# Kernel tuning notes

Measured on AMD Instinct MI355X. Metric: run time of the kernel, lower is better.

Reference implementation:

```python
import jax, jax.numpy as jnp
import numpy as np

B, N = 32, 50000
E = 200000
D, D_LG = 64, 256
M_ALL, M_MEM = 100000, 80000
NUM_VI_SEG = 80000


def _dense(key, din, dout):
    k1, k2 = jax.random.split(key)
    lim = 1.0 / np.sqrt(din)
    W = jax.random.uniform(k1, (din, dout), jnp.float32, -lim, lim)
    b = jax.random.uniform(k2, (dout,), jnp.float32, -lim, lim)
    return W, b


def setup_inputs() -> dict:
    key = jax.random.key(0)
    ks = jax.random.split(key, 16)
    rng = np.random.RandomState(0)

    eg = np.sort(rng.randint(0, B, E)).astype(np.int32)
    vi = rng.randint(0, N, E).astype(np.int32)
    vj = rng.randint(0, N, E).astype(np.int32)
    rel = rng.randint(0, 200, E).astype(np.int32)
    seg_vi = np.sort(rng.randint(0, NUM_VI_SEG, E)).astype(np.int32)
    seg_vj = rng.randint(0, E, E).astype(np.int32)
    e2vi = rng.randint(0, M_ALL, E).astype(np.int32)
    e2vj = rng.randint(0, M_ALL, E).astype(np.int32)
    scanned_edges = jnp.asarray(np.stack([eg, vi, vj, rel, seg_vi, seg_vj, e2vi, e2vj], axis=1))

    new_idx = np.sort(rng.choice(M_ALL, M_MEM, replace=False)).astype(np.int32)[:, None]

    W_h, b_h = _dense(ks[0], D, D)
    W_hlg, b_hlg = _dense(ks[1], D_LG, D)
    W_rlg, b_rlg = _dense(ks[2], D_LG, D)
    Wl0, bl0 = _dense(ks[3], D, D)
    Wr0, br0 = _dense(ks[4], D, D)
    Wl1, bl1 = _dense(ks[5], 2 * D, D)
    Wr1, br1 = _dense(ks[6], 2 * D, D)

    return {
        'node_attention': jax.random.uniform(ks[7], (B, N), jnp.float32),
        'edges_y': jax.random.uniform(ks[8], (E,), jnp.float32),
        'hidden_uncon': jax.random.normal(ks[9], (1, N, D_LG), jnp.float32),
        'hidden_con': jax.random.normal(ks[10], (M_MEM, D), jnp.float32),
        'query_head_emb': jax.random.normal(ks[11], (B, D_LG), jnp.float32),
        'query_rel_emb': jax.random.normal(ks[12], (B, D_LG), jnp.float32),
        'W_h': W_h, 'b_h': b_h, 'W_hlg': W_hlg, 'b_hlg': b_hlg,
        'W_rlg': W_rlg, 'b_rlg': b_rlg,
        'Wl0': Wl0, 'bl0': bl0, 'Wr0': Wr0, 'br0': br0,
        'Wl1': Wl1, 'bl1': bl1, 'Wr1': Wr1, 'br1': br1,
        'scanned_edges': scanned_edges,
        'new_idx_for_memorized': jnp.asarray(new_idx),
        'n_memorized_and_scanned_nodes': M_ALL,
    }


def _segment_softmax(logits, seg, num_seg):
    # numerically-stable sparse softmax over sorted vi-segments
    m = jax.ops.segment_max(logits, seg, num_segments=num_seg)
    e = jnp.exp(logits - m[seg])
    s = jax.ops.segment_sum(e, seg, num_segments=num_seg)
    return e / s[seg]


def reference(node_attention, edges_y, hidden_uncon, hidden_con,
              query_head_emb, query_rel_emb,
              W_h, b_h, W_hlg, b_hlg, W_rlg, b_rlg,
              Wl0, bl0, Wr0, br0, Wl1, bl1, Wr1, br1,
              scanned_edges, new_idx_for_memorized, n_memorized_and_scanned_nodes):
    Bv, Nv = node_attention.shape
    eg = scanned_edges[:, 0]
    vi = scanned_edges[:, 1]
    vj = scanned_edges[:, 2]
    seg_vi = scanned_edges[:, 4]
    e2vi = scanned_edges[:, 6]
    e2vj = scanned_edges[:, 7]

    # proj_for_hidden, scatter memorized states to memorized+scanned slots
    hc = jnp.tanh(hidden_con @ W_h + b_h)                        # M_mem x D
    hc_full = jnp.zeros((n_memorized_and_scanned_nodes, hc.shape[-1]), hc.dtype)
    hc_full = hc_full.at[new_idx_for_memorized[:, 0]].set(hc)    # M_all x D

    hu = jnp.tanh(hidden_uncon @ W_hlg + b_hlg)
    qh = jnp.tanh(query_head_emb @ W_hlg + b_hlg)                # B x D (use_ent_emb)
    qr = jnp.tanh(query_rel_emb @ W_rlg + b_rlg)                 # B x D
    qv = qh + qr

    # node2edge gathers (context = conditioned + unconditioned hidden)
    h_vi = hc_full[e2vi] + hu[0, vi]                             # E x D
    h_vj = hc_full[e2vj] + hu[0, vj]                             # E x D
    q_e = qv[eg]                                                 # E x D

    # transition_fn G with interact [[[0],[1]], [[0,2],[1,2]]]
    l0 = jnp.tanh(h_vi @ Wl0 + bl0)
    r0 = jnp.tanh(h_vj @ Wr0 + br0)
    l1 = jnp.tanh(jnp.concatenate([h_vi, q_e], -1) @ Wl1 + bl1)
    r1 = jnp.tanh(jnp.concatenate([h_vj, q_e], -1) @ Wr1 + br1)
    logits = jnp.sum(l0 * r0, -1) + jnp.sum(l1 * r1, -1)         # E

    # neighbor softmax at vi, modulated by edges_y
    trans = _segment_softmax(logits, seg_vi, NUM_VI_SEG) * edges_y

    # flow: gather attention at vi, aggregate(sum) scatter to (eg_idx, vj)
    flow = node_attention[eg, vi] * trans
    new_att = jnp.zeros((Bv, Nv), flow.dtype).at[eg, vj].add(flow)
    return new_att
```

## Files before the change

### kernel.cpp

```cpp
#include <hip/hip_runtime.h>


typedef __attribute__((ext_vector_type(8))) short s16x8;
typedef __attribute__((ext_vector_type(4))) float f32x4;
typedef __attribute__((ext_vector_type(8))) unsigned short u16x8;

__device__ __forceinline__ float fast_tanh(float x) {
    float e = __expf(2.0f * x);
    return 1.0f - 2.0f * __builtin_amdgcn_rcpf(e + 1.0f);
}

__device__ __forceinline__ unsigned short bf16r(float f) {
    unsigned int u = __float_as_uint(f);
    u = (u + 0x7fffu + ((u >> 16) & 1u)) >> 16;
    return (unsigned short)u;
}
__device__ __forceinline__ float bf16f(unsigned short h) {
    return __uint_as_float(((unsigned int)h) << 16);
}
__device__ __forceinline__ float blo(unsigned int u) {
    return __uint_as_float(u << 16);
}
__device__ __forceinline__ float bhi(unsigned int u) {
    return __uint_as_float(u & 0xffff0000u);
}

__device__ __forceinline__ int saddr(int row, int chunk) {
    return (row << 6) + ((chunk ^ (row & 7)) << 2);
}

__global__ void k_scatter_inv(const int* __restrict__ new_idx, int* __restrict__ inv, int M) {
    int i = blockIdx.x * blockDim.x + threadIdx.x;
    if (i < M) inv[new_idx[i]] = i;
}

__global__ void k_pack(const float* __restrict__ Wl0, const float* __restrict__ Wl1,
                       const float* __restrict__ Wr0, const float* __restrict__ Wr1,
                       unsigned short* __restrict__ Bp) {
    int tid = blockIdx.x * blockDim.x + threadIdx.x;
    if (tid >= 2048) return;
    int lane = tid & 63;
    int ks = (tid >> 6) & 1;
    int g = tid >> 7;
    int col = g * 16 + (lane & 15);
    int kb = ks * 32 + (lane >> 4) * 8;
    const float* W = (col < 64) ? Wl0 : (col < 128) ? Wl1 : (col < 192) ? Wr0 : Wr1;
    int c = col & 63;
    #pragma unroll
    for (int i = 0; i < 8; ++i) {
        float w = W[(kb + i) * 64 + c];
        unsigned short hi = bf16r(w);
        unsigned short lo = bf16r(w - bf16f(hi));
        Bp[(size_t)tid * 8 + i] = hi;
        Bp[16384 + (size_t)tid * 8 + i] = lo;
    }
}

__global__ void k_q(const float* __restrict__ qhe, const float* __restrict__ qre,
                    const float* __restrict__ W_hlg, const float* __restrict__ b_hlg,
                    const float* __restrict__ W_rlg, const float* __restrict__ b_rlg,
                    const float* __restrict__ Wl1, const float* __restrict__ bl1,
                    const float* __restrict__ Wr1, const float* __restrict__ br1,
                    float* __restrict__ ql1b, float* __restrict__ qr1b) {
    __shared__ float qv_s[64];
    int b = blockIdx.x, d = threadIdx.x;
    float ah = 0.f, ar = 0.f;
    for (int k = 0; k < 256; ++k) {
        ah += qhe[b * 256 + k] * W_hlg[k * 64 + d];
        ar += qre[b * 256 + k] * W_rlg[k * 64 + d];
    }
    qv_s[d] = fast_tanh(ah + b_hlg[d]) + fast_tanh(ar + b_rlg[d]);
    __syncthreads();
    float a1 = 0.f, a2 = 0.f;
    for (int k = 0; k < 64; ++k) {
        float v = qv_s[k];
        a1 += v * Wl1[(64 + k) * 64 + d];
        a2 += v * Wr1[(64 + k) * 64 + d];
    }
    ql1b[b * 64 + d] = a1 + bl1[d];
    qr1b[b * 64 + d] = a2 + br1[d];
}

__global__ __launch_bounds__(256, 6) void k_tab(
        const float* __restrict__ Xc, const float* __restrict__ Xu,
        const float* __restrict__ W_h, const float* __restrict__ b_h,
        const float* __restrict__ W_hlg, const float* __restrict__ b_hlg,
        const float* __restrict__ bl0, const float* __restrict__ br0,
        const unsigned short* __restrict__ Bp,
        unsigned short* __restrict__ Ahc, unsigned short* __restrict__ Ahu,
        int M, int N, int HCB) {
    __shared__ float s[64 * 64];
    __shared__ unsigned short dstage[16 * 264];
    unsigned short* hhi = reinterpret_cast<unsigned short*>(s);

    const int t = threadIdx.x;
    const int wu = __builtin_amdgcn_readfirstlane(t >> 6);
    const int lane = t & 63;
    const bool hc = ((int)blockIdx.x < HCB);

    float acc1[16];
    #pragma unroll
    for (int c = 0; c < 16; ++c) acc1[c] = 0.f;

    int base, rows;
    const float* bias;
    unsigned short* table;

    if (hc) {
        base = blockIdx.x * 64;
        rows = (M - base < 64) ? (M - base) : 64;
        bias = b_h;
        table = Ahc;
        #pragma unroll
        for (int i = 0; i < 4; ++i) {
            int f = i * 256 + t;
            int r = f >> 4, ch = f & 15;
            float4 v = make_float4(0.f, 0.f, 0.f, 0.f);
            if (r < rows) v = *reinterpret_cast<const float4*>(Xc + (size_t)(base + r) * 64 + (ch << 2));
            *reinterpret_cast<float4*>(&s[saddr(r, ch)]) = v;
        }
        __syncthreads();
        for (int k4 = 0; k4 < 16; ++k4) {
            float4 xv = *reinterpret_cast<const float4*>(&s[saddr(lane, k4)]);
            #pragma unroll
            for (int kk = 0; kk < 4; ++kk) {
                float xk = (&xv.x)[kk];
                const float* wrow = W_h + (k4 * 4 + kk) * 64 + wu * 16;
                #pragma unroll
                for (int c = 0; c < 16; ++c) acc1[c] = __builtin_fmaf(xk, wrow[c], acc1[c]);
            }
        }
    } else {
        base = ((int)blockIdx.x - HCB) * 64;
        rows = (N - base < 64) ? (N - base) : 64;
        bias = b_hlg;
        table = Ahu;
        float4 xr[4];
        #pragma unroll
        for (int i = 0; i < 4; ++i) {
            int f = i * 256 + t;
            int r = f >> 4, ch = f & 15;
            xr[i] = make_float4(0.f, 0.f, 0.f, 0.f);
            if (r < rows)
                xr[i] = *reinterpret_cast<const float4*>(Xu + (size_t)(base + r) * 256 + (ch << 2));
        }
        for (int kc = 0; kc < 4; ++kc) {
            __syncthreads();
            #pragma unroll
            for (int i = 0; i < 4; ++i) {
                int f = i * 256 + t;
                int r = f >> 4, ch = f & 15;
                *reinterpret_cast<float4*>(&s[saddr(r, ch)]) = xr[i];
            }
            __syncthreads();
            if (kc + 1 < 4) {
                #pragma unroll
                for (int i = 0; i < 4; ++i) {
                    int f = i * 256 + t;
                    int r = f >> 4, ch = f & 15;
                    if (r < rows)
                        xr[i] = *reinterpret_cast<const float4*>(
                            Xu + (size_t)(base + r) * 256 + (kc + 1) * 64 + (ch << 2));
                }
            }
            const float* Wb = W_hlg + (size_t)kc * 64 * 64;
            for (int k4 = 0; k4 < 16; ++k4) {
                float4 xv = *reinterpret_cast<const float4*>(&s[saddr(lane, k4)]);
                #pragma unroll
                for (int kk = 0; kk < 4; ++kk) {
                    float xk = (&xv.x)[kk];
                    const float* wrow = Wb + (k4 * 4 + kk) * 64 + wu * 16;
                    #pragma unroll
                    for (int c = 0; c < 16; ++c) acc1[c] = __builtin_fmaf(xk, wrow[c], acc1[c]);
                }
            }
        }
    }

    __syncthreads();
    {
        unsigned short hi[16];
        #pragma unroll
        for (int c = 0; c < 16; ++c)
            hi[c] = bf16r(fast_tanh(acc1[c] + bias[wu * 16 + c]));
        int o = lane * 68 + wu * 16;
        #pragma unroll
        for (int c = 0; c < 16; ++c) hhi[o + c] = hi[c];
    }
    __syncthreads();

    const s16x8* Bph = reinterpret_cast<const s16x8*>(Bp);
    const s16x8* Bpl = reinterpret_cast<const s16x8*>(Bp + 16384);
    const int l15 = lane & 15, l4 = lane >> 4;
    for (int rt = 0; rt < 4; ++rt) {
        int arow = (rt * 16 + l15) * 68 + l4 * 8;
        s16x8 a0v = *reinterpret_cast<const s16x8*>(&hhi[arow]);
        s16x8 a1v = *reinterpret_cast<const s16x8*>(&hhi[arow + 32]);
        #pragma unroll
        for (int ct = 0; ct < 4; ++ct) {
            int g = wu * 4 + ct;
            s16x8 bh0 = Bph[(g * 2 + 0) * 64 + lane];
            s16x8 bh1 = Bph[(g * 2 + 1) * 64 + lane];
            s16x8 bl0v = Bpl[(g * 2 + 0) * 64 + lane];
            s16x8 bl1v = Bpl[(g * 2 + 1) * 64 + lane];
            f32x4 acc = {0.f, 0.f, 0.f, 0.f};
            acc = __builtin_amdgcn_mfma_f32_16x16x32_bf16(a0v, bh0, acc, 0, 0, 0);
            acc = __builtin_amdgcn_mfma_f32_16x16x32_bf16(a1v, bh1, acc, 0, 0, 0);
            acc = __builtin_amdgcn_mfma_f32_16x16x32_bf16(a0v, bl0v, acc, 0, 0, 0);
            acc = __builtin_amdgcn_mfma_f32_16x16x32_bf16(a1v, bl1v, acc, 0, 0, 0);
            float badd = 0.f;
            if (!hc) {
                if (g < 4) badd = bl0[g * 16 + l15];
                else if (g >= 8 && g < 12) badd = br0[(g - 8) * 16 + l15];
            }
            int side = g >> 3, which = (g >> 2) & 1;
            int x = (g & 3) * 16 + l15;
            int pos = side * 128 + x * 2 + which;
            #pragma unroll
            for (int r = 0; r < 4; ++r)
                dstage[(l4 * 4 + r) * 264 + pos] = bf16r(acc[r] + badd);
        }
        __syncthreads();
        #pragma unroll
        for (int it = 0; it < 2; ++it) {
            int f = (it * 256 + t) * 8;
            int row = f >> 8, off = f & 255;
            u16x8 v = *reinterpret_cast<const u16x8*>(&dstage[row * 264 + off]);
            int grow = rt * 16 + row;
            if (grow < rows)
                *reinterpret_cast<u16x8*>(&table[(size_t)(base + grow) * 256 + off]) = v;
        }
        __syncthreads();
    }
}

__global__ void k_edge(const int* __restrict__ se, const int* __restrict__ inv,
                       const unsigned int* __restrict__ Ahc, const unsigned int* __restrict__ Ahu,
                       const float* __restrict__ ql1b, const float* __restrict__ qr1b,
                       float* __restrict__ trans, float* __restrict__ psum,
                       int E, int ZROW) {
    int tid = blockIdx.x * blockDim.x + threadIdx.x;
    int e = tid >> 4;
    int sl = tid & 15;
    if (e >= E) return;
    const int4* sr = reinterpret_cast<const int4*>(se + (size_t)e * 8);
    int4 ra = sr[0], rb = sr[1];
    int eg = ra.x, vi = ra.y, vj = ra.z, seg = rb.x, e2vi = rb.z, e2vj = rb.w;
    int ii = inv[e2vi]; ii = (ii < 0) ? ZROW : ii;
    int ij = inv[e2vj]; ij = (ij < 0) ? ZROW : ij;
    uint4 a  = *reinterpret_cast<const uint4*>(Ahc + (size_t)ii * 128 + sl * 4);
    uint4 b  = *reinterpret_cast<const uint4*>(Ahu + (size_t)vi * 128 + sl * 4);
    uint4 c  = *reinterpret_cast<const uint4*>(Ahc + (size_t)ij * 128 + 64 + sl * 4);
    uint4 d4 = *reinterpret_cast<const uint4*>(Ahu + (size_t)vj * 128 + 64 + sl * 4);
    float4 q1 = *reinterpret_cast<const float4*>(ql1b + eg * 64 + sl * 4);
    float4 q2 = *reinterpret_cast<const float4*>(qr1b + eg * 64 + sl * 4);
    float acc = 0.f;
    #pragma unroll
    for (int j = 0; j < 4; ++j) {
        unsigned int av = (&a.x)[j], bv = (&b.x)[j];
        unsigned int cv = (&c.x)[j], dv = (&d4.x)[j];
        float l0 = fast_tanh(blo(av) + blo(bv));
        float l1 = fast_tanh(bhi(av) + bhi(bv) + (&q1.x)[j]);
        float r0 = fast_tanh(blo(cv) + blo(dv));
        float r1 = fast_tanh(bhi(cv) + bhi(dv) + (&q2.x)[j]);
        acc = __builtin_fmaf(l0, r0, acc);
        acc = __builtin_fmaf(l1, r1, acc);
    }
    #pragma unroll
    for (int off = 8; off; off >>= 1) acc += __shfl_xor(acc, off);
    if (sl == 0) {
        float ex = __expf(acc);
        trans[e] = ex;
        atomicAdd(&psum[seg], ex);
    }
}

__global__ void k_final(const int* __restrict__ se, const float* __restrict__ trans,
                        const float* __restrict__ psum, const float* __restrict__ ey,
                        const float* __restrict__ natt, float* __restrict__ out,
                        int E, int N) {
    int e = blockIdx.x * blockDim.x + threadIdx.x;
    if (e >= E) return;
    const int* row = se + (size_t)e * 8;
    int eg = row[0], vi = row[1], vj = row[2], seg = row[4];
    float t = trans[e] * __builtin_amdgcn_rcpf(psum[seg]) * ey[e] * natt[(size_t)eg * N + vi];
    atomicAdd(&out[(size_t)eg * N + vj], t);
}

extern "C" void kernel_launch(void* const* d_in, const int* in_sizes, int n_in,
                              void* d_out, int out_size, void* d_ws, size_t ws_size,
                              hipStream_t stream) {
    const float* natt  = (const float*)d_in[0];
    const float* ey    = (const float*)d_in[1];
    const float* h_unc = (const float*)d_in[2];
    const float* h_con = (const float*)d_in[3];
    const float* qhe   = (const float*)d_in[4];
    const float* qre   = (const float*)d_in[5];
    const float* W_h   = (const float*)d_in[6];
    const float* b_h   = (const float*)d_in[7];
    const float* W_hlg = (const float*)d_in[8];
    const float* b_hlg = (const float*)d_in[9];
    const float* W_rlg = (const float*)d_in[10];
    const float* b_rlg = (const float*)d_in[11];
    const float* Wl0   = (const float*)d_in[12];
    const float* bl0   = (const float*)d_in[13];
    const float* Wr0   = (const float*)d_in[14];
    const float* br0   = (const float*)d_in[15];
    const float* Wl1   = (const float*)d_in[16];
    const float* bl1   = (const float*)d_in[17];
    const float* Wr1   = (const float*)d_in[18];
    const float* br1   = (const float*)d_in[19];
    const int* se      = (const int*)d_in[20];
    const int* new_idx = (const int*)d_in[21];

    const int B     = 32;
    const int N     = in_sizes[0] / B;
    const int E     = in_sizes[20] / 8;
    const int M_MEM = in_sizes[21];
    const int M_ALL = 100000;
    const int NSEG  = 80000;

    char* ws = (char*)d_ws;
    size_t off = 0;
    unsigned short* Ahc = (unsigned short*)(ws + off);  off += (size_t)(M_MEM + 1) * 256 * 2;
    unsigned short* Ahu = (unsigned short*)(ws + off);  off += (size_t)N * 256 * 2;
    int* inv = (int*)(ws + off);            off += (size_t)M_ALL * 4;
    float* trans = (float*)(ws + off);      off += (size_t)E * 4;
    float* psum = (float*)(ws + off);       off += (size_t)NSEG * 4;
    float* ql1b = (float*)(ws + off);       off += (size_t)B * 64 * 4;
    float* qr1b = (float*)(ws + off);       off += (size_t)B * 64 * 4;
    unsigned short* Bpack = (unsigned short*)(ws + off); off += (size_t)2 * 16384 * 2;

    hipMemsetAsync(d_out, 0, (size_t)out_size * 4, stream);
    hipMemsetAsync(inv, 0xFF, (size_t)M_ALL * 4, stream);
    hipMemsetAsync(psum, 0, (size_t)NSEG * 4, stream);
    hipMemsetAsync(Ahc + (size_t)M_MEM * 256, 0, 256 * 2, stream);

    const int HCB = (M_MEM + 63) / 64;
    const int HUB = (N + 63) / 64;

    k_scatter_inv<<<(M_MEM + 255) / 256, 256, 0, stream>>>(new_idx, inv, M_MEM);
    k_pack<<<8, 256, 0, stream>>>(Wl0, Wl1, Wr0, Wr1, Bpack);
    k_q<<<B, 64, 0, stream>>>(qhe, qre, W_hlg, b_hlg, W_rlg, b_rlg,
                              Wl1, bl1, Wr1, br1, ql1b, qr1b);
    k_tab<<<HCB + HUB, 256, 0, stream>>>(h_con, h_unc, W_h, b_h, W_hlg, b_hlg,
                                         bl0, br0, Bpack, Ahc, Ahu, M_MEM, N, HCB);
    k_edge<<<((size_t)E * 16 + 255) / 256, 256, 0, stream>>>(se, inv, (const unsigned int*)Ahc,
                                                (const unsigned int*)Ahu, ql1b, qr1b,
                                                trans, psum, E, M_MEM);
    k_final<<<(E + 255) / 256, 256, 0, stream>>>(se, trans, psum, ey, natt, (float*)d_out, E, N);
}
```

Measured before the change: 141.7 us.

## Move edge-weight gathers into edge kernel and batch LDS loads in table GEMM

The edge kernel now multiplies the exponentiated logit by edges_y and the gathered node attention, and writes a compact (output index, segment) pair per edge. The final kernel then reads only that pair, the partial value and the segment sum, and no longer re-reads the 32-byte edge row or does the random node-attention gather. The first-stage GEMM in the table kernel also loads four LDS rows at once before the FMAs, to give the scheduler more independent loads. In exchange the edge kernel does an extra scattered gather and writes an additional 8-byte array per edge.

```diff
diff --git a/kernel.cpp b/kernel.cpp
--- a/kernel.cpp
+++ b/kernel.cpp
@@ -81,6 +81,25 @@
     qr1b[b * 64 + d] = a2 + br1[d];
 }
 
+__device__ __forceinline__ void s1_batch(const float* __restrict__ s, int lane, int b4,
+                                         const float* __restrict__ Wbase, int wu,
+                                         float acc1[16]) {
+    f32x4 xrow[4];
+    #pragma unroll
+    for (int j = 0; j < 4; ++j)
+        xrow[j] = *reinterpret_cast<const f32x4*>(&s[saddr(lane, b4 * 4 + j)]);
+    #pragma unroll
+    for (int k4 = 0; k4 < 4; ++k4) {
+        #pragma unroll
+        for (int kk = 0; kk < 4; ++kk) {
+            float xk = xrow[k4][kk];
+            const float* wrow = Wbase + ((b4 * 4 + k4) * 4 + kk) * 64 + wu * 16;
+            #pragma unroll
+            for (int c = 0; c < 16; ++c) acc1[c] = __builtin_fmaf(xk, wrow[c], acc1[c]);
+        }
+    }
+}
+
 __global__ __launch_bounds__(256, 6) void k_tab(
         const float* __restrict__ Xc, const float* __restrict__ Xu,
         const float* __restrict__ W_h, const float* __restrict__ b_h,
@@ -120,16 +139,8 @@
             *reinterpret_cast<float4*>(&s[saddr(r, ch)]) = v;
         }
         __syncthreads();
-        for (int k4 = 0; k4 < 16; ++k4) {
-            float4 xv = *reinterpret_cast<const float4*>(&s[saddr(lane, k4)]);
-            #pragma unroll
-            for (int kk = 0; kk < 4; ++kk) {
-                float xk = (&xv.x)[kk];
-                const float* wrow = W_h + (k4 * 4 + kk) * 64 + wu * 16;
-                #pragma unroll
-                for (int c = 0; c < 16; ++c) acc1[c] = __builtin_fmaf(xk, wrow[c], acc1[c]);
-            }
-        }
+        for (int b4 = 0; b4 < 4; ++b4)
+            s1_batch(s, lane, b4, W_h, wu, acc1);
     } else {
         base = ((int)blockIdx.x - HCB) * 64;
         rows = (N - base < 64) ? (N - base) : 64;
@@ -164,16 +175,8 @@
                 }
             }
             const float* Wb = W_hlg + (size_t)kc * 64 * 64;
-            for (int k4 = 0; k4 < 16; ++k4) {
-                float4 xv = *reinterpret_cast<const float4*>(&s[saddr(lane, k4)]);
-                #pragma unroll
-                for (int kk = 0; kk < 4; ++kk) {
-                    float xk = (&xv.x)[kk];
-                    const float* wrow = Wb + (k4 * 4 + kk) * 64 + wu * 16;
-                    #pragma unroll
-                    for (int c = 0; c < 16; ++c) acc1[c] = __builtin_fmaf(xk, wrow[c], acc1[c]);
-                }
-            }
+            for (int b4 = 0; b4 < 4; ++b4)
+                s1_batch(s, lane, b4, Wb, wu, acc1);
         }
     }
 
@@ -237,8 +240,9 @@
 __global__ void k_edge(const int* __restrict__ se, const int* __restrict__ inv,
                        const unsigned int* __restrict__ Ahc, const unsigned int* __restrict__ Ahu,
                        const float* __restrict__ ql1b, const float* __restrict__ qr1b,
+                       const float* __restrict__ ey, const float* __restrict__ natt,
                        float* __restrict__ trans, float* __restrict__ psum,
-                       int E, int ZROW) {
+                       int2* __restrict__ aux, int E, int N, int ZROW) {
     int tid = blockIdx.x * blockDim.x + threadIdx.x;
     int e = tid >> 4;
     int sl = tid & 15;
@@ -270,21 +274,19 @@
     for (int off = 8; off; off >>= 1) acc += __shfl_xor(acc, off);
     if (sl == 0) {
         float ex = __expf(acc);
-        trans[e] = ex;
+        trans[e] = ex * ey[e] * natt[(size_t)eg * N + vi];
+        aux[e] = make_int2(eg * N + vj, seg);
         atomicAdd(&psum[seg], ex);
     }
 }
 
-__global__ void k_final(const int* __restrict__ se, const float* __restrict__ trans,
-                        const float* __restrict__ psum, const float* __restrict__ ey,
-                        const float* __restrict__ natt, float* __restrict__ out,
-                        int E, int N) {
+__global__ void k_final(const int2* __restrict__ aux, const float* __restrict__ trans,
+                        const float* __restrict__ psum, float* __restrict__ out, int E) {
     int e = blockIdx.x * blockDim.x + threadIdx.x;
     if (e >= E) return;
-    const int* row = se + (size_t)e * 8;
-    int eg = row[0], vi = row[1], vj = row[2], seg = row[4];
-    float t = trans[e] * __builtin_amdgcn_rcpf(psum[seg]) * ey[e] * natt[(size_t)eg * N + vi];
-    atomicAdd(&out[(size_t)eg * N + vj], t);
+    int2 a = aux[e];
+    float t = trans[e] * __builtin_amdgcn_rcpf(psum[a.y]);
+    atomicAdd(&out[a.x], t);
 }
 
 extern "C" void kernel_launch(void* const* d_in, const int* in_sizes, int n_in,
@@ -327,6 +329,7 @@
     int* inv = (int*)(ws + off);            off += (size_t)M_ALL * 4;
     float* trans = (float*)(ws + off);      off += (size_t)E * 4;
     float* psum = (float*)(ws + off);       off += (size_t)NSEG * 4;
+    int2* aux = (int2*)(ws + off);          off += (size_t)E * 8;
     float* ql1b = (float*)(ws + off);       off += (size_t)B * 64 * 4;
     float* qr1b = (float*)(ws + off);       off += (size_t)B * 64 * 4;
     unsigned short* Bpack = (unsigned short*)(ws + off); off += (size_t)2 * 16384 * 2;
@@ -347,6 +350,6 @@
                                          bl0, br0, Bpack, Ahc, Ahu, M_MEM, N, HCB);
     k_edge<<<((size_t)E * 16 + 255) / 256, 256, 0, stream>>>(se, inv, (const unsigned int*)Ahc,
                                                 (const unsigned int*)Ahu, ql1b, qr1b,
-                                                trans, psum, E, M_MEM);
-    k_final<<<(E + 255) / 256, 256, 0, stream>>>(se, trans, psum, ey, natt, (float*)d_out, E, N);
-}
+                                                ey, natt, trans, psum, aux, E, N, M_MEM);
+    k_final<<<(E + 255) / 256, 256, 0, stream>>>(aux, trans, psum, (float*)d_out, E);
+}
```

Result: no change. 142.0 us (+0.2%).
